# Kernel tuning notes

Measured on AMD Instinct MI355X. Metric: run time of the kernel, lower is better.

## Reference

```python
import jax, jax.numpy as jnp
import numpy as np

B = 128          # number of trees
DEPTH = 8        # complete binary tree depth -> 2^8-1 nodes per tree
NPT = 2 ** DEPTH - 1          # 255 nodes per tree
N = B * NPT                   # 32640 total nodes
E_T = NPT - 1                 # 254 edges per tree
F_IN = 64
H = 256


def _build_trees():
    """Complete binary trees; children of local node i are 2i+1, 2i+2."""
    idx = np.arange(NPT)
    depth = np.floor(np.log2(idx + 1)).astype(np.int64)
    order = (DEPTH - 1) - depth                 # leaves=0, root=DEPTH-1
    internal = idx[: NPT // 2]                  # nodes that have children
    parents = np.repeat(internal, 2)
    children = np.empty_like(parents)
    children[0::2] = 2 * internal + 1
    children[1::2] = 2 * internal + 2
    adj_local = np.stack([parents, children], axis=1)        # [E_T, 2]
    offs = (np.arange(B) * NPT)[:, None, None]
    adjacency = (adj_local[None, :, :] + offs).reshape(-1, 2)  # [B*E_T, 2]
    node_order = np.tile(order, B)                             # [N]
    edge_order = np.tile(order[parents], B)                    # [B*E_T]
    return node_order, adjacency, edge_order


def setup_inputs() -> dict:
    key = jax.random.key(0)
    ks = jax.random.split(key, 8)
    node_order, adjacency_list, edge_order = _build_trees()
    s = lambda k, shape, fan: jax.random.normal(k, shape, jnp.float32) * (fan ** -0.5)
    return {
        "features": jax.random.normal(ks[0], (N, F_IN), jnp.float32),
        "node_order": jnp.asarray(node_order, jnp.int32),
        "adjacency_list": jnp.asarray(adjacency_list, jnp.int32),
        "edge_order": jnp.asarray(edge_order, jnp.int32),
        "W_iou_w": s(ks[1], (3 * H, F_IN), F_IN),
        "W_iou_b": jnp.zeros((3 * H,), jnp.float32),
        "U_iou_w": s(ks[2], (3 * H, H), H),
        "W_f_w": s(ks[3], (H, F_IN), F_IN),
        "W_f_b": jnp.zeros((H,), jnp.float32),
        "U_f_w": s(ks[4], (H, H), H),
        "lin0_w": s(ks[5], (H, H), H),
        "lin0_b": jnp.zeros((H,), jnp.float32),
        "lin1_w": s(ks[6], (1, H), H),
        "lin1_b": jnp.zeros((1,), jnp.float32),
    }


def reference(features, node_order, adjacency_list, edge_order,
              W_iou_w, W_iou_b, U_iou_w, W_f_w, W_f_b, U_f_w,
              lin0_w, lin0_b, lin1_w, lin1_b):
    n = features.shape[0]
    parent = adjacency_list[:, 0]
    child = adjacency_list[:, 1]
    # input->gate projections, computed once for all nodes
    wx_iou = features @ W_iou_w.T + W_iou_b      # [N, 3H]
    wx_f = features @ W_f_w.T + W_f_b            # [N, H]
    h = jnp.zeros((n, H), features.dtype)
    c = jnp.zeros((n, H), features.dtype)
    # sequential bottom-up sweep over topological levels (static DEPTH levels)
    for t in range(DEPTH):
        nmask = (node_order == t)[:, None]
        emask = (edge_order == t).astype(features.dtype)[:, None]
        child_h = h[child]                       # [E, H] gather
        h_sum = jax.ops.segment_sum(child_h * emask, parent, num_segments=n)
        iou = wx_iou + h_sum @ U_iou_w.T         # [N, 3H]; h_sum==0 at level 0
        i, o, u = jnp.split(iou, 3, axis=1)
        i = jax.nn.sigmoid(i); o = jax.nn.sigmoid(o); u = jnp.tanh(u)
        f = jax.nn.sigmoid(wx_f[parent] + child_h @ U_f_w.T)  # [E, H]
        c_sum = jax.ops.segment_sum(f * c[child] * emask, parent, num_segments=n)
        new_c = i * u + c_sum
        new_h = o * jnp.tanh(new_c)
        h = jnp.where(nmask, new_h, h)
        c = jnp.where(nmask, new_c, c)
    # unbatch + mean-pool per tree (use_root=False); equal-size trees -> reshape
    x = h.reshape(B, NPT, H).mean(axis=1)        # [B, H]
    # MLP head: Linear -> ReLU -> (dropout inactive in eval) -> Linear
    x = x @ lin0_w.T + lin0_b
    x = jax.nn.relu(x)
    x = x @ lin1_w.T + lin1_b                    # [B, 1]
    return x.reshape(-1)                         # flattened, aux output is None
```

## Files before the change

kernel.cpp:

```cpp
#include <hip/hip_runtime.h>

#define B_TREES 128
#define NPT 255
#define NTOT (B_TREES * NPT)
#define FIN 64
#define HH 256

typedef short bf16x8 __attribute__((ext_vector_type(8)));
typedef float f32x4  __attribute__((ext_vector_type(4)));
typedef unsigned short u16;

__device__ __forceinline__ float sigf(float x) {
    return __frcp_rn(1.0f + __expf(-x));
}
__device__ __forceinline__ float tanh_fast(float x) {
    return __builtin_fmaf(2.0f, sigf(2.0f * x), -1.0f);
}
__device__ __forceinline__ u16 bf_hi(float v) {
    unsigned u = __float_as_uint(v);
    return (u16)((u + 0x7FFFu + ((u >> 16) & 1u)) >> 16);
}
__device__ __forceinline__ float bf_f(u16 b) { return __uint_as_float(((unsigned)b) << 16); }

__global__ __launch_bounds__(256) void pack_B(
    const float* __restrict__ Uiou, const float* __restrict__ Uf,
    const float* __restrict__ Wiou, const float* __restrict__ Wf,
    u16* __restrict__ Bhi, u16* __restrict__ Blo, float* __restrict__ WxT)
{
    int idx = blockIdx.x * 256 + threadIdx.x;
    if (idx < 409600) {
        int j    = idx & 7;
        int lane = (idx >> 3) & 63;
        int ksl  = (idx >> 9) % 10;
        int ct   = idx / 5120;
        int s = ct % 5, hb = ct / 5;
        int n = lane & 15, q = lane >> 4;
        int jH = hb * 16 + n;
        int k = (s < 4 ? ksl * 32 : 320 + ksl * 32) + q * 8 + j;
        float v = 0.0f;
        if (s == 4) {
            if (k < 576) v = Uf[(size_t)jH * HH + (k - 320)];
        } else {
            if (k < 256) {
                v = (s < 3) ? Uiou[(size_t)(s * 256 + jH) * HH + k]
                            : Uf[(size_t)jH * HH + k];
            } else {
                int kw = k - 256;
                v = (s < 3) ? Wiou[(size_t)(s * 256 + jH) * FIN + kw]
                            : 2.0f * Wf[(size_t)jH * FIN + kw];
            }
        }
        u16 hi = bf_hi(v);
        u16 lo = bf_hi(v - bf_f(hi));
        Bhi[idx] = hi;
        Blo[idx] = lo;
    } else {
        int idx2 = idx - 409600;
        int k = idx2 >> 10, j = idx2 & 1023;
        float v = (j < 768) ? Wiou[(size_t)j * 64 + k] : 2.0f * Wf[(size_t)(j - 768) * 64 + k];
        WxT[(size_t)(k >> 2) * 4096 + j * 4 + (k & 3)] = v;
    }
}

__global__ __launch_bounds__(256) void leaf_v2(
    const float* __restrict__ feat,
    const float* __restrict__ WxT, const float* __restrict__ biou,
    float* __restrict__ h, float* __restrict__ c)
{
    const int NB = 8;
    __shared__ float xs[NB][FIN];
    int tid = threadIdx.x;
    int l0 = blockIdx.x * NB;
    int b = l0 >> 7;
    int g0 = b * NPT + 127 + (l0 & 127);
    const float* fb = feat + (size_t)g0 * FIN;
    for (int i = tid; i < NB * FIN; i += 256) ((float*)xs)[i] = fb[i];
    __syncthreads();

    float ai[NB], ao[NB], au[NB];
#pragma unroll
    for (int n = 0; n < NB; ++n) { ai[n] = 0.f; ao[n] = 0.f; au[n] = 0.f; }

    const float4* WxT4 = (const float4*)WxT;
    for (int k4 = 0; k4 < 16; ++k4) {
        size_t base = (size_t)k4 * 1024 + tid;
        float4 wi = WxT4[base], wo = WxT4[base + 256], wu = WxT4[base + 512];
#pragma unroll
        for (int n = 0; n < NB; ++n) {
            float4 x4 = ((const float4*)xs[n])[k4];
            ai[n] += wi.x * x4.x + wi.y * x4.y + wi.z * x4.z + wi.w * x4.w;
            ao[n] += wo.x * x4.x + wo.y * x4.y + wo.z * x4.z + wo.w * x4.w;
            au[n] += wu.x * x4.x + wu.y * x4.y + wu.z * x4.z + wu.w * x4.w;
        }
    }

    float bi = biou[tid], bo = biou[tid + 256], bu = biou[tid + 512];
#pragma unroll
    for (int n = 0; n < NB; ++n) {
        float iv = sigf(ai[n] + bi);
        float ov = sigf(ao[n] + bo);
        float uv = tanh_fast(au[n] + bu);
        float cv = iv * uv;
        float hv = ov * tanh_fast(cv);
        c[(size_t)(g0 + n) * HH + tid] = cv;
        h[(size_t)(g0 + n) * HH + tid] = hv;
    }
}

template<int NCT>
__global__ __launch_bounds__(256, 2) void level_mfma(
    const float* __restrict__ feat,
    const u16* __restrict__ Bhi, const u16* __restrict__ Blo,
    const float* __restrict__ biou, const float* __restrict__ bfv,
    float* __restrict__ h, float* __restrict__ c,
    int Lt, int lg)
{
    constexpr int CSPLIT = 20 / NCT;
    constexpr int SUBS = NCT / 5;
    __shared__ char smem[73728];
    short* Ahi = (short*)smem;
    short* Alo = (short*)(smem + 36864);

    const int tid = threadIdx.x;
    const int lane = tid & 63, w = tid >> 6;
    const int cs = blockIdx.x % CSPLIT;
    const int rb = blockIdx.x / CSPLIT;
    const int m0 = rb * 32;
    const int msk = (1 << lg) - 1;
    const int ctbase = cs * 4 * NCT + w * NCT;

    const float4* Hf4 = (const float4*)h;
    const float4* Ff4 = (const float4*)feat;

    for (int rep = 0; rep < 8; ++rep) {
        int flat = rep * 256 + tid;
        int m = flat >> 6, f4 = flat & 63;
        int mg = m0 + m;
        int b = mg >> lg, ii = Lt + (mg & msk);
        int gc = b * NPT + 2 * ii + 1;
        float4 h1 = Hf4[(size_t)gc * 64 + f4];
        float4 h2 = Hf4[(size_t)(gc + 1) * 64 + f4];
        float hsv[4] = {h1.x + h2.x, h1.y + h2.y, h1.z + h2.z, h1.w + h2.w};
        float hdv[4] = {h1.x - h2.x, h1.y - h2.y, h1.z - h2.z, h1.w - h2.w};
        int rt = m >> 4, lm = m & 15;
        int ks = f4 >> 3;
        int lane_ = lm + 16 * ((f4 >> 1) & 3);
        int j0 = (f4 & 1) * 4;
        ushort4 sh, sl, dh, dl;
        u16* shp = (u16*)&sh; u16* slp = (u16*)&sl;
        u16* dhp = (u16*)&dh; u16* dlp = (u16*)&dl;
#pragma unroll
        for (int e = 0; e < 4; ++e) {
            u16 a = bf_hi(hsv[e]); shp[e] = a; slp[e] = bf_hi(hsv[e] - bf_f(a));
            u16 d = bf_hi(hdv[e]); dhp[e] = d; dlp[e] = bf_hi(hdv[e] - bf_f(d));
        }
        int base_s = ((rt * 18 + ks) * 64 + lane_) * 8 + j0;
        int base_d = ((rt * 18 + ks + 10) * 64 + lane_) * 8 + j0;
        *(ushort4*)&Ahi[base_s] = sh;  *(ushort4*)&Alo[base_s] = sl;
        *(ushort4*)&Ahi[base_d] = dh;  *(ushort4*)&Alo[base_d] = dl;
    }
    for (int rep = 0; rep < 2; ++rep) {
        int flat = rep * 256 + tid;
        int m = flat >> 4, f4 = flat & 15;
        int mg = m0 + m;
        int b = mg >> lg, ii = Lt + (mg & msk);
        int g = b * NPT + ii;
        float4 x4 = Ff4[(size_t)g * 16 + f4];
        float xv[4] = {x4.x, x4.y, x4.z, x4.w};
        int rt = m >> 4, lm = m & 15;
        int ks = 8 + (f4 >> 3);
        int lane_ = lm + 16 * ((f4 >> 1) & 3);
        int j0 = (f4 & 1) * 4;
        ushort4 xh, xl;
        u16* xhp = (u16*)&xh; u16* xlp = (u16*)&xl;
#pragma unroll
        for (int e = 0; e < 4; ++e) {
            u16 a = bf_hi(xv[e]); xhp[e] = a; xlp[e] = bf_hi(xv[e] - bf_f(a));
        }
        int base = ((rt * 18 + ks) * 64 + lane_) * 8 + j0;
        *(ushort4*)&Ahi[base] = xh;  *(ushort4*)&Alo[base] = xl;
    }
    __syncthreads();

    f32x4 acc[2][NCT];
#pragma unroll
    for (int rt = 0; rt < 2; ++rt)
#pragma unroll
        for (int i = 0; i < NCT; ++i) acc[rt][i] = (f32x4){0.f, 0.f, 0.f, 0.f};

    for (int G = 0; G < 10; ++G) {
        bf16x8 ah[2], al[2];
#pragma unroll
        for (int rt = 0; rt < 2; ++rt) {
            ah[rt] = *(const bf16x8*)&Ahi[((rt * 18 + G) * 64 + lane) * 8];
            al[rt] = *(const bf16x8*)&Alo[((rt * 18 + G) * 64 + lane) * 8];
        }
#pragma unroll
        for (int ctl = 0; ctl < NCT; ++ctl) {
            if (ctl % 5 == 4) continue;
            size_t slot = (size_t)((ctbase + ctl) * 10 + G) * 512 + lane * 8;
            bf16x8 bh = *(const bf16x8*)(Bhi + slot);
            bf16x8 bl = *(const bf16x8*)(Blo + slot);
#pragma unroll
            for (int rt = 0; rt < 2; ++rt) {
                acc[rt][ctl] = __builtin_amdgcn_mfma_f32_16x16x32_bf16(ah[rt], bh, acc[rt][ctl], 0, 0, 0);
                acc[rt][ctl] = __builtin_amdgcn_mfma_f32_16x16x32_bf16(ah[rt], bl, acc[rt][ctl], 0, 0, 0);
                acc[rt][ctl] = __builtin_amdgcn_mfma_f32_16x16x32_bf16(al[rt], bh, acc[rt][ctl], 0, 0, 0);
            }
        }
    }
    for (int G = 10; G < 18; ++G) {
        bf16x8 ah[2], al[2];
#pragma unroll
        for (int rt = 0; rt < 2; ++rt) {
            ah[rt] = *(const bf16x8*)&Ahi[((rt * 18 + G) * 64 + lane) * 8];
            al[rt] = *(const bf16x8*)&Alo[((rt * 18 + G) * 64 + lane) * 8];
        }
#pragma unroll
        for (int ctl = 4; ctl < NCT; ctl += 5) {
            size_t slot = (size_t)((ctbase + ctl) * 10 + (G - 10)) * 512 + lane * 8;
            bf16x8 bh = *(const bf16x8*)(Bhi + slot);
            bf16x8 bl = *(const bf16x8*)(Blo + slot);
#pragma unroll
            for (int rt = 0; rt < 2; ++rt) {
                acc[rt][ctl] = __builtin_amdgcn_mfma_f32_16x16x32_bf16(ah[rt], bh, acc[rt][ctl], 0, 0, 0);
                acc[rt][ctl] = __builtin_amdgcn_mfma_f32_16x16x32_bf16(ah[rt], bl, acc[rt][ctl], 0, 0, 0);
                acc[rt][ctl] = __builtin_amdgcn_mfma_f32_16x16x32_bf16(al[rt], bh, acc[rt][ctl], 0, 0, 0);
            }
        }
    }
    __syncthreads();

    float* sc = (float*)smem + w * 2592;
    const int n = lane & 15, q = lane >> 4;
#pragma unroll
    for (int sub = 0; sub < SUBS; ++sub) {
#pragma unroll
        for (int rt = 0; rt < 2; ++rt)
#pragma unroll
            for (int s = 0; s < 5; ++s) {
                f32x4 v = acc[rt][sub * 5 + s];
#pragma unroll
                for (int r = 0; r < 4; ++r)
                    sc[(rt * 16 + q * 4 + r) * 81 + s * 16 + n] = v[r];
            }
        int hb_abs = ctbase / 5 + sub;
        int jHb = hb_abs * 16;
        for (int it = 0; it < 8; ++it) {
            int idx = it * 64 + lane;
            int m = idx >> 4, jl = idx & 15;
            int jH = jHb + jl;
            float Ci  = sc[m * 81 + jl];
            float Co  = sc[m * 81 + 16 + jl];
            float Cu  = sc[m * 81 + 32 + jl];
            float Cfs = sc[m * 81 + 48 + jl];
            float Cfd = sc[m * 81 + 64 + jl];
            int mg = m0 + m;
            int b = mg >> lg, ii = Lt + (mg & msk);
            size_t g = (size_t)b * NPT + ii;
            float iv = sigf(Ci + biou[jH]);
            float ov = sigf(Co + biou[256 + jH]);
            float uv = tanh_fast(Cu + biou[512 + jH]);
            size_t gc = g + ii + 1;
            float bF = bfv[jH];
            float f1 = sigf(0.5f * (Cfs + Cfd) + bF);
            float f2 = sigf(0.5f * (Cfs - Cfd) + bF);
            float cv = iv * uv + f1 * c[gc * HH + jH] + f2 * c[(gc + 1) * HH + jH];
            float hv = ov * tanh_fast(cv);
            c[g * HH + jH] = cv;
            h[g * HH + jH] = hv;
        }
    }
}

__global__ __launch_bounds__(256) void head_partial(
    const float* __restrict__ h, float* __restrict__ hp)
{
    int blk = blockIdx.x;
    int b = blk >> 3, p = blk & 7, tid = threadIdx.x;
    const float* hb = h + ((size_t)b * NPT + p * 32) * HH;
    int rows = (p == 7) ? 31 : 32;
    float a0 = 0.f, a1 = 0.f, a2 = 0.f, a3 = 0.f;
    int i = 0;
    for (; i + 3 < rows; i += 4) {
        a0 += hb[(size_t)(i + 0) * HH + tid];
        a1 += hb[(size_t)(i + 1) * HH + tid];
        a2 += hb[(size_t)(i + 2) * HH + tid];
        a3 += hb[(size_t)(i + 3) * HH + tid];
    }
    for (; i < rows; ++i) a0 += hb[(size_t)i * HH + tid];
    hp[(size_t)blk * HH + tid] = a0 + a1 + a2 + a3;
}

__global__ __launch_bounds__(256) void head_final(
    const float* __restrict__ hp,
    const float* __restrict__ l0w, const float* __restrict__ l0b,
    const float* __restrict__ l1w, const float* __restrict__ l1b,
    float* __restrict__ out)
{
    __shared__ float ms[HH];
    __shared__ float red[4];
    int b = blockIdx.x, tid = threadIdx.x;
    float a = 0.f;
#pragma unroll
    for (int p = 0; p < 8; ++p) a += hp[(size_t)(b * 8 + p) * HH + tid];
    ms[tid] = a * (1.0f / (float)NPT);
    __syncthreads();

    const float4* L0 = (const float4*)(l0w + (size_t)tid * HH);
    float y = 0.f;
    for (int k4 = 0; k4 < 64; ++k4) {
        float4 wv = L0[k4];
        float4 m4 = ((const float4*)ms)[k4];
        y += wv.x * m4.x + wv.y * m4.y + wv.z * m4.z + wv.w * m4.w;
    }
    y += l0b[tid];
    y = fmaxf(y, 0.f);
    float v = y * l1w[tid];
    for (int off = 32; off > 0; off >>= 1) v += __shfl_down(v, off, 64);
    if ((tid & 63) == 0) red[tid >> 6] = v;
    __syncthreads();
    if (tid == 0) out[b] = red[0] + red[1] + red[2] + red[3] + l1b[0];
}

extern "C" void kernel_launch(void* const* d_in, const int* in_sizes, int n_in,
                              void* d_out, int out_size, void* d_ws, size_t ws_size,
                              hipStream_t stream)
{
    const float* feat = (const float*)d_in[0];
    const float* Wiou = (const float*)d_in[4];
    const float* biou = (const float*)d_in[5];
    const float* Uiou = (const float*)d_in[6];
    const float* Wf   = (const float*)d_in[7];
    const float* bfv  = (const float*)d_in[8];
    const float* Uf   = (const float*)d_in[9];
    const float* l0w  = (const float*)d_in[10];
    const float* l0b  = (const float*)d_in[11];
    const float* l1w  = (const float*)d_in[12];
    const float* l1b  = (const float*)d_in[13];

    float* h  = (float*)d_ws;
    float* c  = h + (size_t)NTOT * HH;
    u16* Bhi  = (u16*)(c + (size_t)NTOT * HH);
    u16* Blo  = Bhi + 409600;
    float* WxT = (float*)(Blo + 409600);
    float* hp  = WxT + 65536;

    pack_B<<<1856, 256, 0, stream>>>(Uiou, Uf, Wiou, Wf, Bhi, Blo, WxT);

    leaf_v2<<<2048, 256, 0, stream>>>(feat, WxT, biou, h, c);
    level_mfma<5><<<1024, 256, 0, stream>>>(feat, Bhi, Blo, biou, bfv, h, c, 63, 6);
    level_mfma<5><<<512, 256, 0, stream>>>(feat, Bhi, Blo, biou, bfv, h, c, 31, 5);
    level_mfma<5><<<256, 256, 0, stream>>>(feat, Bhi, Blo, biou, bfv, h, c, 15, 4);
    level_mfma<5><<<128, 256, 0, stream>>>(feat, Bhi, Blo, biou, bfv, h, c, 7, 3);
    level_mfma<5><<<64, 256, 0, stream>>>(feat, Bhi, Blo, biou, bfv, h, c, 3, 2);
    level_mfma<5><<<32, 256, 0, stream>>>(feat, Bhi, Blo, biou, bfv, h, c, 1, 1);
    level_mfma<5><<<16, 256, 0, stream>>>(feat, Bhi, Blo, biou, bfv, h, c, 0, 0);

    head_partial<<<1024, 256, 0, stream>>>(h, hp);
    head_final<<<B_TREES, 256, 0, stream>>>(hp, l0w, l0b, l1w, l1b, (float*)d_out);
}
```

Measured before the change: 297.1 us.

## Fuse level kernels and head into persistent megakernel with grid barriers

Replaces the seven per-level launches and the two head kernels with one persistent 512-block kernel. The levels are separated by atomic-counter grid barriers, and pack_B now zeroes the counters. The first level switches to level_body<10> so 512 blocks cover it, giving each block more column tiles. The aim is to remove launch and drain gaps between the small late-level kernels. The cost is spin-wait barriers, a hard co-residency requirement (512 blocks at two per CU), idle blocks on the small levels, and possible deadlock if not all blocks are resident.

```diff
diff --git a/kernel.cpp b/kernel.cpp
--- a/kernel.cpp
+++ b/kernel.cpp
@@ -22,10 +22,22 @@
 }
 __device__ __forceinline__ float bf_f(u16 b) { return __uint_as_float(((unsigned)b) << 16); }
 
+__device__ __forceinline__ void gbar(unsigned* cnt) {
+    __syncthreads();
+    if (threadIdx.x == 0) {
+        __threadfence();
+        atomicAdd(cnt, 1u);
+        while (atomicAdd(cnt, 0u) < 512u) __builtin_amdgcn_s_sleep(8);
+        __threadfence();
+    }
+    __syncthreads();
+}
+
 __global__ __launch_bounds__(256) void pack_B(
     const float* __restrict__ Uiou, const float* __restrict__ Uf,
     const float* __restrict__ Wiou, const float* __restrict__ Wf,
-    u16* __restrict__ Bhi, u16* __restrict__ Blo, float* __restrict__ WxT)
+    u16* __restrict__ Bhi, u16* __restrict__ Blo, float* __restrict__ WxT,
+    unsigned* __restrict__ cnt)
 {
     int idx = blockIdx.x * 256 + threadIdx.x;
     if (idx < 409600) {
@@ -56,9 +68,13 @@
         Blo[idx] = lo;
     } else {
         int idx2 = idx - 409600;
-        int k = idx2 >> 10, j = idx2 & 1023;
-        float v = (j < 768) ? Wiou[(size_t)j * 64 + k] : 2.0f * Wf[(size_t)(j - 768) * 64 + k];
-        WxT[(size_t)(k >> 2) * 4096 + j * 4 + (k & 3)] = v;
+        if (idx2 < 65536) {
+            int k = idx2 >> 10, j = idx2 & 1023;
+            float v = (j < 768) ? Wiou[(size_t)j * 64 + k] : 2.0f * Wf[(size_t)(j - 768) * 64 + k];
+            WxT[(size_t)(k >> 2) * 4096 + j * 4 + (k & 3)] = v;
+        } else if (idx2 < 65536 + 32) {
+            cnt[idx2 - 65536] = 0u;
+        }
     }
 }
 
@@ -108,7 +124,8 @@
 }
 
 template<int NCT>
-__global__ __launch_bounds__(256, 2) void level_mfma(
+__device__ void level_body(
+    int bid, char* smem,
     const float* __restrict__ feat,
     const u16* __restrict__ Bhi, const u16* __restrict__ Blo,
     const float* __restrict__ biou, const float* __restrict__ bfv,
@@ -117,14 +134,13 @@
 {
     constexpr int CSPLIT = 20 / NCT;
     constexpr int SUBS = NCT / 5;
-    __shared__ char smem[73728];
     short* Ahi = (short*)smem;
     short* Alo = (short*)(smem + 36864);
 
     const int tid = threadIdx.x;
     const int lane = tid & 63, w = tid >> 6;
-    const int cs = blockIdx.x % CSPLIT;
-    const int rb = blockIdx.x / CSPLIT;
+    const int cs = bid % CSPLIT;
+    const int rb = bid / CSPLIT;
     const int m0 = rb * 32;
     const int msk = (1 << lg) - 1;
     const int ctbase = cs * 4 * NCT + w * NCT;
@@ -273,54 +289,75 @@
     }
 }
 
-__global__ __launch_bounds__(256) void head_partial(
-    const float* __restrict__ h, float* __restrict__ hp)
-{
-    int blk = blockIdx.x;
-    int b = blk >> 3, p = blk & 7, tid = threadIdx.x;
-    const float* hb = h + ((size_t)b * NPT + p * 32) * HH;
-    int rows = (p == 7) ? 31 : 32;
-    float a0 = 0.f, a1 = 0.f, a2 = 0.f, a3 = 0.f;
-    int i = 0;
-    for (; i + 3 < rows; i += 4) {
-        a0 += hb[(size_t)(i + 0) * HH + tid];
-        a1 += hb[(size_t)(i + 1) * HH + tid];
-        a2 += hb[(size_t)(i + 2) * HH + tid];
-        a3 += hb[(size_t)(i + 3) * HH + tid];
-    }
-    for (; i < rows; ++i) a0 += hb[(size_t)i * HH + tid];
-    hp[(size_t)blk * HH + tid] = a0 + a1 + a2 + a3;
-}
-
-__global__ __launch_bounds__(256) void head_final(
-    const float* __restrict__ hp,
+__global__ __launch_bounds__(256, 2) void mega(
+    const float* __restrict__ feat,
+    const u16* __restrict__ Bhi, const u16* __restrict__ Blo,
+    const float* __restrict__ biou, const float* __restrict__ bfv,
+    float* __restrict__ h, float* __restrict__ c, float* __restrict__ hp,
     const float* __restrict__ l0w, const float* __restrict__ l0b,
     const float* __restrict__ l1w, const float* __restrict__ l1b,
-    float* __restrict__ out)
-{
-    __shared__ float ms[HH];
-    __shared__ float red[4];
-    int b = blockIdx.x, tid = threadIdx.x;
-    float a = 0.f;
-#pragma unroll
-    for (int p = 0; p < 8; ++p) a += hp[(size_t)(b * 8 + p) * HH + tid];
-    ms[tid] = a * (1.0f / (float)NPT);
-    __syncthreads();
-
-    const float4* L0 = (const float4*)(l0w + (size_t)tid * HH);
-    float y = 0.f;
-    for (int k4 = 0; k4 < 64; ++k4) {
-        float4 wv = L0[k4];
-        float4 m4 = ((const float4*)ms)[k4];
-        y += wv.x * m4.x + wv.y * m4.y + wv.z * m4.z + wv.w * m4.w;
-    }
-    y += l0b[tid];
-    y = fmaxf(y, 0.f);
-    float v = y * l1w[tid];
-    for (int off = 32; off > 0; off >>= 1) v += __shfl_down(v, off, 64);
-    if ((tid & 63) == 0) red[tid >> 6] = v;
-    __syncthreads();
-    if (tid == 0) out[b] = red[0] + red[1] + red[2] + red[3] + l1b[0];
+    float* __restrict__ out, unsigned* __restrict__ cnt)
+{
+    __shared__ char smem[73728];
+    const int bid = blockIdx.x;
+    const int tid = threadIdx.x;
+
+    level_body<10>(bid, smem, feat, Bhi, Blo, biou, bfv, h, c, 63, 6);
+    gbar(cnt + 0);
+    level_body<5>(bid, smem, feat, Bhi, Blo, biou, bfv, h, c, 31, 5);
+    gbar(cnt + 1);
+    if (bid < 256) level_body<5>(bid, smem, feat, Bhi, Blo, biou, bfv, h, c, 15, 4);
+    gbar(cnt + 2);
+    if (bid < 128) level_body<5>(bid, smem, feat, Bhi, Blo, biou, bfv, h, c, 7, 3);
+    gbar(cnt + 3);
+    if (bid < 64) level_body<5>(bid, smem, feat, Bhi, Blo, biou, bfv, h, c, 3, 2);
+    gbar(cnt + 4);
+    if (bid < 32) level_body<5>(bid, smem, feat, Bhi, Blo, biou, bfv, h, c, 1, 1);
+    gbar(cnt + 5);
+    if (bid < 16) level_body<5>(bid, smem, feat, Bhi, Blo, biou, bfv, h, c, 0, 0);
+    gbar(cnt + 6);
+
+    {
+        int b = bid >> 2, p = bid & 3;
+        const float* hbp = h + ((size_t)b * NPT + p * 64) * HH;
+        int rows = (p == 3) ? 63 : 64;
+        float a0 = 0.f, a1 = 0.f, a2 = 0.f, a3 = 0.f;
+        int i = 0;
+        for (; i + 3 < rows; i += 4) {
+            a0 += hbp[(size_t)(i + 0) * HH + tid];
+            a1 += hbp[(size_t)(i + 1) * HH + tid];
+            a2 += hbp[(size_t)(i + 2) * HH + tid];
+            a3 += hbp[(size_t)(i + 3) * HH + tid];
+        }
+        for (; i < rows; ++i) a0 += hbp[(size_t)i * HH + tid];
+        hp[(size_t)bid * HH + tid] = a0 + a1 + a2 + a3;
+    }
+    gbar(cnt + 7);
+
+    if (bid < 128) {
+        float* ms  = (float*)smem;
+        float* red = ms + HH;
+        float a = 0.f;
+#pragma unroll
+        for (int p = 0; p < 4; ++p) a += hp[(size_t)(bid * 4 + p) * HH + tid];
+        ms[tid] = a * (1.0f / (float)NPT);
+        __syncthreads();
+
+        const float4* L0 = (const float4*)(l0w + (size_t)tid * HH);
+        float y = 0.f;
+        for (int k4 = 0; k4 < 64; ++k4) {
+            float4 wv = L0[k4];
+            float4 m4 = ((const float4*)ms)[k4];
+            y += wv.x * m4.x + wv.y * m4.y + wv.z * m4.z + wv.w * m4.w;
+        }
+        y += l0b[tid];
+        y = fmaxf(y, 0.f);
+        float v = y * l1w[tid];
+        for (int off = 32; off > 0; off >>= 1) v += __shfl_down(v, off, 64);
+        if ((tid & 63) == 0) red[tid >> 6] = v;
+        __syncthreads();
+        if (tid == 0) out[bid] = red[0] + red[1] + red[2] + red[3] + l1b[0];
+    }
 }
 
 extern "C" void kernel_launch(void* const* d_in, const int* in_sizes, int n_in,
@@ -339,24 +376,18 @@
     const float* l1w  = (const float*)d_in[12];
     const float* l1b  = (const float*)d_in[13];
 
-    float* h  = (float*)d_ws;
-    float* c  = h + (size_t)NTOT * HH;
-    u16* Bhi  = (u16*)(c + (size_t)NTOT * HH);
-    u16* Blo  = Bhi + 409600;
+    float* h   = (float*)d_ws;
+    float* c   = h + (size_t)NTOT * HH;
+    u16* Bhi   = (u16*)(c + (size_t)NTOT * HH);
+    u16* Blo   = Bhi + 409600;
     float* WxT = (float*)(Blo + 409600);
     float* hp  = WxT + 65536;
-
-    pack_B<<<1856, 256, 0, stream>>>(Uiou, Uf, Wiou, Wf, Bhi, Blo, WxT);
+    unsigned* cnt = (unsigned*)(hp + 512 * 256);
+
+    pack_B<<<1857, 256, 0, stream>>>(Uiou, Uf, Wiou, Wf, Bhi, Blo, WxT, cnt);
 
     leaf_v2<<<2048, 256, 0, stream>>>(feat, WxT, biou, h, c);
-    level_mfma<5><<<1024, 256, 0, stream>>>(feat, Bhi, Blo, biou, bfv, h, c, 63, 6);
-    level_mfma<5><<<512, 256, 0, stream>>>(feat, Bhi, Blo, biou, bfv, h, c, 31, 5);
-    level_mfma<5><<<256, 256, 0, stream>>>(feat, Bhi, Blo, biou, bfv, h, c, 15, 4);
-    level_mfma<5><<<128, 256, 0, stream>>>(feat, Bhi, Blo, biou, bfv, h, c, 7, 3);
-    level_mfma<5><<<64, 256, 0, stream>>>(feat, Bhi, Blo, biou, bfv, h, c, 3, 2);
-    level_mfma<5><<<32, 256, 0, stream>>>(feat, Bhi, Blo, biou, bfv, h, c, 1, 1);
-    level_mfma<5><<<16, 256, 0, stream>>>(feat, Bhi, Blo, biou, bfv, h, c, 0, 0);
-
-    head_partial<<<1024, 256, 0, stream>>>(h, hp);
-    head_final<<<B_TREES, 256, 0, stream>>>(hp, l0w, l0b, l1w, l1b, (float*)d_out);
-}
+
+    mega<<<512, 256, 0, stream>>>(feat, Bhi, Blo, biou, bfv, h, c, hp,
+                                  l0w, l0b, l1w, l1b, (float*)d_out, cnt);
+}
```

Result: slower. 598.2 us (+101.4%).
